# Performance work log

Hardware: AMD Instinct MI355X
Metric: run time of the kernel (lower is better)

## Reference

```python
import jax, jax.numpy as jnp
import numpy as np

B, N, M, G = 2, 8192, 8192, 256
X_MIN = Y_MIN = -35.0
CELL = abs(2.0 * X_MIN / G)  # cell size, as in construct_batched_cuda_grid


def setup_inputs() -> dict:
    key = jax.random.key(0)
    k1, k2, k3, k4, k5 = jax.random.split(key, 5)
    p_i = jax.random.uniform(k1, (B, N, 3), jnp.float32, -34.0, 34.0)
    p_j = jax.random.uniform(k2, (B, M, 3), jnp.float32, -34.0, 34.0)
    mos = jax.random.normal(k3, (B, 2, G, G), jnp.float32)
    error_p_i_flow = jax.random.uniform(k4, (B, N), jnp.float32)
    nearest_flow = jax.random.randint(k5, (B, N, 1), 0, M, jnp.int32)
    return {"p_i": p_i, "mos": mos, "p_j": p_j,
            "error_p_i_flow": error_p_i_flow, "nearest_flow": nearest_flow}


def _knn1_l1(x, y):
    # brute-force 1-NN with L1 (norm=1) distance, matching knn_points(..., K=1, norm=1)
    # build (B,N,M) dist one coordinate at a time to avoid a (B,N,M,3) intermediate
    d = (jnp.abs(x[:, :, None, 0] - y[:, None, :, 0])
         + jnp.abs(x[:, :, None, 1] - y[:, None, :, 1])
         + jnp.abs(x[:, :, None, 2] - y[:, None, :, 2]))
    return jnp.min(d, axis=-1), jnp.argmin(d, axis=-1)


def reference(p_i, mos, p_j, error_p_i_flow, nearest_flow):
    # NN_loss with reduction='none' -> error_p_i_rigid = (cham_x + cham_y)/2 (needs N==M)
    cham_x, nearest_rigid = _knn1_l1(p_i, p_j)  # (B,N), (B,N)
    cham_y, _ = _knn1_l1(p_j, p_i)              # (B,M)
    error_p_i_rigid = (cham_x + cham_y) * 0.5

    dynamic = error_p_i_flow > error_p_i_rigid             # (B,N) bool
    idx = jnp.where(dynamic, nearest_flow[..., 0], nearest_rigid)  # (B,N)
    art_labels = dynamic.astype(jnp.int32)                 # (B,N) in {0,1}

    # batched gather p_j[b, idx[b]]
    p_j_by_nn = jnp.take_along_axis(p_j, idx[..., None], axis=1)  # (B,N,3)

    # construct_batched_cuda_grid: scatter labels into (B,G,G), -1 elsewhere
    shift = jnp.array([X_MIN, Y_MIN], jnp.float32)
    cell_idx = ((p_j_by_nn[:, :, :2] - shift) / CELL).astype(jnp.int32)  # (B,N,2)
    bs = jnp.repeat(jnp.arange(B), N)
    grid = -jnp.ones((B, G, G), jnp.int32)
    grid = grid.at[bs,
                   cell_idx[..., 0].reshape(-1),
                   cell_idx[..., 1].reshape(-1)].set(art_labels.reshape(-1))

    # CrossEntropyLoss(ignore_index=-1), mean over non-ignored cells
    logp = jax.nn.log_softmax(mos, axis=1)                 # (B,C,G,G)
    valid = grid >= 0
    tgt = jnp.clip(grid, 0, None)
    lp = jnp.take_along_axis(logp, tgt[:, None], axis=1)[:, 0]  # (B,G,G)
    loss = -jnp.where(valid, lp, 0.0).sum() / jnp.maximum(valid.sum(), 1).astype(lp.dtype)
    return loss
```

## Files before the change

### kernel.cpp

```cpp
#include <hip/hip_runtime.h>
#include <float.h>

#define B_ 2
#define N_ 8192
#define G_ 256
constexpr float X_MIN_F = -35.0f;
constexpr float CELL_F  = 0.2734375f;

using u64 = unsigned long long;

#define OFF_ACCUM 524288
#define OFF_PX    524352

template<int CC>
__global__ __launch_bounds__(256) void nn_kernel(const float* __restrict__ p_i,
                                                 const float* __restrict__ p_j,
                                                 u64* __restrict__ px,
                                                 float* __restrict__ py,
                                                 int* __restrict__ grid,
                                                 unsigned* __restrict__ accum)
{
    constexpr int COLS = N_ / CC;
    constexpr int NB   = 32 * CC;
    const int dir  = blockIdx.z >> 1;
    const int b    = blockIdx.z & 1;
    const int tid  = threadIdx.x;
    const int row0 = blockIdx.x * 1024 + tid * 4;
    const int c0   = blockIdx.y * COLS;

    const float* __restrict__ P = dir ? p_j : p_i;
    const float* __restrict__ Q = dir ? p_i : p_j;

    __shared__ __align__(16) float q[COLS * 3];
    for (int t = tid; t < COLS * 3 / 4; t += 256)
        ((float4*)q)[t] = ((const float4*)(Q + ((size_t)b * N_ + c0) * 3))[t];

    {
        const int lin = blockIdx.x + 8 * (blockIdx.y + CC * blockIdx.z);
        constexpr int PER = 32768 / NB;
        if (tid < PER)
            ((uint4*)grid)[lin * PER + tid] = make_uint4(~0u, ~0u, ~0u, ~0u);
        if (lin == 0 && tid < 4) accum[tid] = 0u;
    }

    const float4* pp = (const float4*)(P + ((size_t)b * N_ + row0) * 3);
    float4 r0 = pp[0], r1 = pp[1], r2 = pp[2];
    float px_[4] = {r0.x, r0.w, r1.z, r2.y};
    float py_[4] = {r0.y, r1.x, r1.w, r2.z};
    float pz_[4] = {r0.z, r1.y, r2.x, r2.w};

    float best[4];
#pragma unroll
    for (int r = 0; r < 4; r++) best[r] = FLT_MAX;

    __syncthreads();

    if (dir == 0) {
        int gcol[4] = {0, 0, 0, 0};
        for (int jg = 0; jg < COLS; jg += 8) {
            const float4* qv = (const float4*)&q[jg * 3];
            float4 v0 = qv[0], v1 = qv[1], v2 = qv[2];
            float4 v3 = qv[3], v4 = qv[4], v5 = qv[5];
            float qx[8] = {v0.x, v0.w, v1.z, v2.y, v3.x, v3.w, v4.z, v5.y};
            float qy[8] = {v0.y, v1.x, v1.w, v2.z, v3.y, v4.x, v4.w, v5.z};
            float qz[8] = {v0.z, v1.y, v2.x, v2.w, v3.z, v4.y, v5.x, v5.w};
#pragma unroll
            for (int r = 0; r < 4; r++) {
                float d[8];
#pragma unroll
                for (int k = 0; k < 8; k++)
                    d[k] = (fabsf(px_[r] - qx[k]) + fabsf(py_[r] - qy[k]))
                           + fabsf(pz_[r] - qz[k]);
                float m01 = fminf(d[0], d[1]), m23 = fminf(d[2], d[3]);
                float m45 = fminf(d[4], d[5]), m67 = fminf(d[6], d[7]);
                float m = fminf(fminf(m01, m23), fminf(m45, m67));
                bool lt = m < best[r];
                best[r] = lt ? m : best[r];
                gcol[r] = lt ? jg : gcol[r];
            }
        }
        int bidx[4];
#pragma unroll
        for (int r = 0; r < 4; r++) {
            const float4* qv = (const float4*)&q[gcol[r] * 3];
            float4 v0 = qv[0], v1 = qv[1], v2 = qv[2];
            float4 v3 = qv[3], v4 = qv[4], v5 = qv[5];
            float qx[8] = {v0.x, v0.w, v1.z, v2.y, v3.x, v3.w, v4.z, v5.y};
            float qy[8] = {v0.y, v1.x, v1.w, v2.z, v3.y, v4.x, v4.w, v5.z};
            float qz[8] = {v0.z, v1.y, v2.x, v2.w, v3.z, v4.y, v5.x, v5.w};
            int kk = 0;
#pragma unroll
            for (int k = 7; k >= 0; k--) {
                float d = (fabsf(px_[r] - qx[k]) + fabsf(py_[r] - qy[k]))
                          + fabsf(pz_[r] - qz[k]);
                kk = (d == best[r]) ? k : kk;
            }
            bidx[r] = c0 + gcol[r] + kk;
        }
        const size_t o = (size_t)blockIdx.y * (B_ * N_) + b * N_ + row0;
#pragma unroll
        for (int r = 0; r < 4; r++)
            px[o + r] = ((u64)__float_as_uint(best[r]) << 32) | (unsigned)bidx[r];
    } else {
        for (int jg = 0; jg < COLS; jg += 8) {
            const float4* qv = (const float4*)&q[jg * 3];
            float4 v0 = qv[0], v1 = qv[1], v2 = qv[2];
            float4 v3 = qv[3], v4 = qv[4], v5 = qv[5];
            float qx[8] = {v0.x, v0.w, v1.z, v2.y, v3.x, v3.w, v4.z, v5.y};
            float qy[8] = {v0.y, v1.x, v1.w, v2.z, v3.y, v4.x, v4.w, v5.z};
            float qz[8] = {v0.z, v1.y, v2.x, v2.w, v3.z, v4.y, v5.x, v5.w};
#pragma unroll
            for (int r = 0; r < 4; r++) {
#pragma unroll
                for (int k = 0; k < 8; k++) {
                    float d = (fabsf(px_[r] - qx[k]) + fabsf(py_[r] - qy[k]))
                              + fabsf(pz_[r] - qz[k]);
                    best[r] = fminf(best[r], d);
                }
            }
        }
        const size_t o = (size_t)blockIdx.y * (B_ * N_) + b * N_ + row0;
#pragma unroll
        for (int r = 0; r < 4; r++) py[o + r] = best[r];
    }
}

template<int CC>
__global__ __launch_bounds__(256) void reduce_scatter_kernel(
    const u64* __restrict__ px, const float* __restrict__ py,
    const float* __restrict__ flow, const int* __restrict__ nflow,
    const float* __restrict__ Pj, int* __restrict__ grid)
{
    __shared__ u64      sbx[64];
    __shared__ unsigned sby[64];
    const int tid = threadIdx.x;
    const int p   = tid & 63;
    const int g   = tid >> 6;
    constexpr int CPG = CC / 4;

    if (tid < 64) { sbx[tid] = ~0ull; sby[tid] = ~0u; }
    __syncthreads();

    const int pt = blockIdx.x * 64 + p;
    u64   bx = ~0ull;
    float by = FLT_MAX;
#pragma unroll
    for (int k = 0; k < CPG; k++) {
        int c = g * CPG + k;
        u64 v = px[(size_t)c * (B_ * N_) + pt];
        bx = v < bx ? v : bx;
        by = fminf(by, py[(size_t)c * (B_ * N_) + pt]);
    }
    atomicMin(&sbx[p], bx);
    atomicMin(&sby[p], __float_as_uint(by));
    __syncthreads();

    if (tid < 64) {
        u64 fx = sbx[tid];
        float dx = __uint_as_float((unsigned)(fx >> 32));
        float dy = __uint_as_float(sby[tid]);
        float rigid = (dx + dy) * 0.5f;

        const int i = blockIdx.x * 64 + tid;
        const int b = i >> 13;
        const int n = i & (N_ - 1);

        bool dyn  = flow[i] > rigid;
        int label = dyn ? 1 : 0;
        int idx   = dyn ? nflow[i] : (int)(unsigned)(fx & 0xFFFFFFFFull);

        const float* qp = Pj + ((size_t)b * N_ + idx) * 3;
        float xx = qp[0], yy = qp[1];

        int cx = (int)((xx - X_MIN_F) / CELL_F);
        int cy = (int)((yy - X_MIN_F) / CELL_F);

        atomicMax(&grid[(b << 16) + cx * G_ + cy], (n << 1) | label);
    }
}

__global__ __launch_bounds__(256) void ce_kernel(const float* __restrict__ mos,
                                                 const int* __restrict__ grid,
                                                 float* __restrict__ accum,
                                                 float* __restrict__ out)
{
    int i = blockIdx.x * 256 + threadIdx.x;
    float lsum = 0.0f;
    int   lcnt = 0;

    int packed = grid[i];
    if (packed >= 0) {
        int b    = i >> 16;
        int cell = i & 0xFFFF;
        float m0 = mos[((size_t)b * 2 + 0) * 65536 + cell];
        float m1 = mos[((size_t)b * 2 + 1) * 65536 + cell];
        float mx = fmaxf(m0, m1);
        float lse = logf(expf(m0 - mx) + expf(m1 - mx));
        float sh  = ((packed & 1) ? m1 : m0) - mx;
        lsum = sh - lse;
        lcnt = 1;
    }

#pragma unroll
    for (int o = 32; o > 0; o >>= 1) {
        lsum += __shfl_down(lsum, o);
        lcnt += __shfl_down(lcnt, o);
    }
    __shared__ float wsum[4];
    __shared__ int   wcnt[4];
    int wave = threadIdx.x >> 6;
    if ((threadIdx.x & 63) == 0) { wsum[wave] = lsum; wcnt[wave] = lcnt; }
    __syncthreads();
    if (threadIdx.x == 0) {
        float s = wsum[0] + wsum[1] + wsum[2] + wsum[3];
        int   c = wcnt[0] + wcnt[1] + wcnt[2] + wcnt[3];
        atomicAdd(&accum[0], s);
        atomicAdd((int*)&accum[1], c);
        __threadfence();
        unsigned t = atomicAdd((unsigned*)&accum[2], 1u);
        if (t == gridDim.x - 1) {
            float S = atomicAdd(&accum[0], 0.0f);
            int   C = atomicAdd((int*)&accum[1], 0);
            out[0] = -S / (float)(C > 0 ? C : 1);
        }
    }
}

template<int CC>
static void run(const float* p_i, const float* mos, const float* p_j,
                const float* flow, const int* nflow, float* out,
                char* ws, hipStream_t stream)
{
    int*   grid  = (int*)ws;
    float* accum = (float*)(ws + OFF_ACCUM);
    u64*   px    = (u64*)(ws + OFF_PX);
    float* py    = (float*)(ws + OFF_PX + (size_t)CC * B_ * N_ * 8);

    dim3 g(8, CC, 4);
    nn_kernel<CC><<<g, 256, 0, stream>>>(p_i, p_j, px, py, (int*)grid,
                                         (unsigned*)accum);
    reduce_scatter_kernel<CC><<<256, 256, 0, stream>>>(px, py, flow, nflow,
                                                       p_j, grid);
    ce_kernel<<<(B_ * G_ * G_) / 256, 256, 0, stream>>>(mos, grid, accum, out);
}

extern "C" void kernel_launch(void* const* d_in, const int* in_sizes, int n_in,
                              void* d_out, int out_size, void* d_ws, size_t ws_size,
                              hipStream_t stream)
{
    const float* p_i   = (const float*)d_in[0];
    const float* mos   = (const float*)d_in[1];
    const float* p_j   = (const float*)d_in[2];
    const float* flow  = (const float*)d_in[3];
    const int*   nflow = (const int*)d_in[4];
    float* out = (float*)d_out;
    char* ws = (char*)d_ws;

    if (ws_size >= OFF_PX + (size_t)64 * B_ * N_ * 12)
        run<64>(p_i, mos, p_j, flow, nflow, out, ws, stream);
    else if (ws_size >= OFF_PX + (size_t)32 * B_ * N_ * 12)
        run<32>(p_i, mos, p_j, flow, nflow, out, ws, stream);
    else
        run<8>(p_i, mos, p_j, flow, nflow, out, ws, stream);
}
```

Measured before the change: 128.4 us.

## Use packed float2 math and 8 rows per thread in NN kernel

The brute-force L1 nearest-neighbour kernel now gives each thread 8 query rows instead of 4, which halves the number of row blocks and gets more reuse from each shared-memory column load. The distance math uses 2-wide float vectors so the compiler can emit packed FP32 instructions (v_pk_add/min style) on CDNA. The reduce-scatter kernel is rebalanced to 16 points per block with more column groups per point, and the fallback CC becomes 16 so the smaller grid still divides evenly. The cost is higher register pressure from 8 rows and vector accumulators, plus fewer blocks in the NN launch, which may lower occupancy.

```diff
diff --git a/kernel.cpp b/kernel.cpp
--- a/kernel.cpp
+++ b/kernel.cpp
@@ -8,9 +8,14 @@
 constexpr float CELL_F  = 0.2734375f;
 
 using u64 = unsigned long long;
+typedef float v2f __attribute__((ext_vector_type(2)));
 
 #define OFF_ACCUM 524288
 #define OFF_PX    524352
+
+__device__ __forceinline__ v2f vabs2(v2f x) {
+    return __builtin_elementwise_max(x, -x);
+}
 
 template<int CC>
 __global__ __launch_bounds__(256) void nn_kernel(const float* __restrict__ p_i,
@@ -21,11 +26,11 @@
                                                  unsigned* __restrict__ accum)
 {
     constexpr int COLS = N_ / CC;
-    constexpr int NB   = 32 * CC;
+    constexpr int NB   = 16 * CC;
     const int dir  = blockIdx.z >> 1;
     const int b    = blockIdx.z & 1;
     const int tid  = threadIdx.x;
-    const int row0 = blockIdx.x * 1024 + tid * 4;
+    const int row0 = blockIdx.x * 2048 + tid * 8;
     const int c0   = blockIdx.y * COLS;
 
     const float* __restrict__ P = dir ? p_j : p_i;
@@ -36,52 +41,62 @@
         ((float4*)q)[t] = ((const float4*)(Q + ((size_t)b * N_ + c0) * 3))[t];
 
     {
-        const int lin = blockIdx.x + 8 * (blockIdx.y + CC * blockIdx.z);
+        const int lin = blockIdx.x + 4 * (blockIdx.y + CC * blockIdx.z);
         constexpr int PER = 32768 / NB;
-        if (tid < PER)
-            ((uint4*)grid)[lin * PER + tid] = make_uint4(~0u, ~0u, ~0u, ~0u);
+        for (int t = tid; t < PER; t += 256)
+            ((uint4*)grid)[lin * PER + t] = make_uint4(~0u, ~0u, ~0u, ~0u);
         if (lin == 0 && tid < 4) accum[tid] = 0u;
     }
 
-    const float4* pp = (const float4*)(P + ((size_t)b * N_ + row0) * 3);
-    float4 r0 = pp[0], r1 = pp[1], r2 = pp[2];
-    float px_[4] = {r0.x, r0.w, r1.z, r2.y};
-    float py_[4] = {r0.y, r1.x, r1.w, r2.z};
-    float pz_[4] = {r0.z, r1.y, r2.x, r2.w};
-
-    float best[4];
-#pragma unroll
-    for (int r = 0; r < 4; r++) best[r] = FLT_MAX;
+    float px_[8], py_[8], pz_[8];
+    {
+        const float4* pp = (const float4*)(P + ((size_t)b * N_ + row0) * 3);
+        float4 v0 = pp[0], v1 = pp[1], v2 = pp[2];
+        float4 v3 = pp[3], v4 = pp[4], v5 = pp[5];
+        float X[8] = {v0.x, v0.w, v1.z, v2.y, v3.x, v3.w, v4.z, v5.y};
+        float Y[8] = {v0.y, v1.x, v1.w, v2.z, v3.y, v4.x, v4.w, v5.z};
+        float Z[8] = {v0.z, v1.y, v2.x, v2.w, v3.z, v4.y, v5.x, v5.w};
+#pragma unroll
+        for (int r = 0; r < 8; r++) { px_[r] = X[r]; py_[r] = Y[r]; pz_[r] = Z[r]; }
+    }
 
     __syncthreads();
 
     if (dir == 0) {
-        int gcol[4] = {0, 0, 0, 0};
+        float best[8]; int gcol[8];
+#pragma unroll
+        for (int r = 0; r < 8; r++) { best[r] = FLT_MAX; gcol[r] = 0; }
+
         for (int jg = 0; jg < COLS; jg += 8) {
             const float4* qv = (const float4*)&q[jg * 3];
             float4 v0 = qv[0], v1 = qv[1], v2 = qv[2];
             float4 v3 = qv[3], v4 = qv[4], v5 = qv[5];
-            float qx[8] = {v0.x, v0.w, v1.z, v2.y, v3.x, v3.w, v4.z, v5.y};
-            float qy[8] = {v0.y, v1.x, v1.w, v2.z, v3.y, v4.x, v4.w, v5.z};
-            float qz[8] = {v0.z, v1.y, v2.x, v2.w, v3.z, v4.y, v5.x, v5.w};
-#pragma unroll
-            for (int r = 0; r < 4; r++) {
-                float d[8];
-#pragma unroll
-                for (int k = 0; k < 8; k++)
-                    d[k] = (fabsf(px_[r] - qx[k]) + fabsf(py_[r] - qy[k]))
-                           + fabsf(pz_[r] - qz[k]);
-                float m01 = fminf(d[0], d[1]), m23 = fminf(d[2], d[3]);
-                float m45 = fminf(d[4], d[5]), m67 = fminf(d[6], d[7]);
-                float m = fminf(fminf(m01, m23), fminf(m45, m67));
+            v2f qx2[4] = {{v0.x, v0.w}, {v1.z, v2.y}, {v3.x, v3.w}, {v4.z, v5.y}};
+            v2f qy2[4] = {{v0.y, v1.x}, {v1.w, v2.z}, {v3.y, v4.x}, {v4.w, v5.z}};
+            v2f qz2[4] = {{v0.z, v1.y}, {v2.x, v2.w}, {v3.z, v4.y}, {v5.x, v5.w}};
+#pragma unroll
+            for (int r = 0; r < 8; r++) {
+                v2f P2x = {px_[r], px_[r]};
+                v2f P2y = {py_[r], py_[r]};
+                v2f P2z = {pz_[r], pz_[r]};
+                v2f s[4];
+#pragma unroll
+                for (int t = 0; t < 4; t++) {
+                    s[t] = (vabs2(P2x - qx2[t]) + vabs2(P2y - qy2[t]))
+                           + vabs2(P2z - qz2[t]);
+                }
+                v2f m2 = __builtin_elementwise_min(
+                             __builtin_elementwise_min(s[0], s[1]),
+                             __builtin_elementwise_min(s[2], s[3]));
+                float m = fminf(m2.x, m2.y);
                 bool lt = m < best[r];
                 best[r] = lt ? m : best[r];
                 gcol[r] = lt ? jg : gcol[r];
             }
         }
-        int bidx[4];
-#pragma unroll
-        for (int r = 0; r < 4; r++) {
+        const size_t o = (size_t)blockIdx.y * (B_ * N_) + b * N_ + row0;
+#pragma unroll
+        for (int r = 0; r < 8; r++) {
             const float4* qv = (const float4*)&q[gcol[r] * 3];
             float4 v0 = qv[0], v1 = qv[1], v2 = qv[2];
             float4 v3 = qv[3], v4 = qv[4], v5 = qv[5];
@@ -95,33 +110,37 @@
                           + fabsf(pz_[r] - qz[k]);
                 kk = (d == best[r]) ? k : kk;
             }
-            bidx[r] = c0 + gcol[r] + kk;
-        }
-        const size_t o = (size_t)blockIdx.y * (B_ * N_) + b * N_ + row0;
-#pragma unroll
-        for (int r = 0; r < 4; r++)
-            px[o + r] = ((u64)__float_as_uint(best[r]) << 32) | (unsigned)bidx[r];
+            int bidx = c0 + gcol[r] + kk;
+            px[o + r] = ((u64)__float_as_uint(best[r]) << 32) | (unsigned)bidx;
+        }
     } else {
+        v2f bm[8];
+#pragma unroll
+        for (int r = 0; r < 8; r++) bm[r] = (v2f){FLT_MAX, FLT_MAX};
+
         for (int jg = 0; jg < COLS; jg += 8) {
             const float4* qv = (const float4*)&q[jg * 3];
             float4 v0 = qv[0], v1 = qv[1], v2 = qv[2];
             float4 v3 = qv[3], v4 = qv[4], v5 = qv[5];
-            float qx[8] = {v0.x, v0.w, v1.z, v2.y, v3.x, v3.w, v4.z, v5.y};
-            float qy[8] = {v0.y, v1.x, v1.w, v2.z, v3.y, v4.x, v4.w, v5.z};
-            float qz[8] = {v0.z, v1.y, v2.x, v2.w, v3.z, v4.y, v5.x, v5.w};
-#pragma unroll
-            for (int r = 0; r < 4; r++) {
-#pragma unroll
-                for (int k = 0; k < 8; k++) {
-                    float d = (fabsf(px_[r] - qx[k]) + fabsf(py_[r] - qy[k]))
-                              + fabsf(pz_[r] - qz[k]);
-                    best[r] = fminf(best[r], d);
+            v2f qx2[4] = {{v0.x, v0.w}, {v1.z, v2.y}, {v3.x, v3.w}, {v4.z, v5.y}};
+            v2f qy2[4] = {{v0.y, v1.x}, {v1.w, v2.z}, {v3.y, v4.x}, {v4.w, v5.z}};
+            v2f qz2[4] = {{v0.z, v1.y}, {v2.x, v2.w}, {v3.z, v4.y}, {v5.x, v5.w}};
+#pragma unroll
+            for (int r = 0; r < 8; r++) {
+                v2f P2x = {px_[r], px_[r]};
+                v2f P2y = {py_[r], py_[r]};
+                v2f P2z = {pz_[r], pz_[r]};
+#pragma unroll
+                for (int t = 0; t < 4; t++) {
+                    v2f s = (vabs2(P2x - qx2[t]) + vabs2(P2y - qy2[t]))
+                            + vabs2(P2z - qz2[t]);
+                    bm[r] = __builtin_elementwise_min(bm[r], s);
                 }
             }
         }
         const size_t o = (size_t)blockIdx.y * (B_ * N_) + b * N_ + row0;
 #pragma unroll
-        for (int r = 0; r < 4; r++) py[o + r] = best[r];
+        for (int r = 0; r < 8; r++) py[o + r] = fminf(bm[r].x, bm[r].y);
     }
 }
 
@@ -131,17 +150,17 @@
     const float* __restrict__ flow, const int* __restrict__ nflow,
     const float* __restrict__ Pj, int* __restrict__ grid)
 {
-    __shared__ u64      sbx[64];
-    __shared__ unsigned sby[64];
+    __shared__ u64      sbx[16];
+    __shared__ unsigned sby[16];
     const int tid = threadIdx.x;
-    const int p   = tid & 63;
-    const int g   = tid >> 6;
-    constexpr int CPG = CC / 4;
-
-    if (tid < 64) { sbx[tid] = ~0ull; sby[tid] = ~0u; }
-    __syncthreads();
-
-    const int pt = blockIdx.x * 64 + p;
+    const int p   = tid & 15;
+    const int g   = tid >> 4;
+    constexpr int CPG = CC / 16;
+
+    if (tid < 16) { sbx[tid] = ~0ull; sby[tid] = ~0u; }
+    __syncthreads();
+
+    const int pt = blockIdx.x * 16 + p;
     u64   bx = ~0ull;
     float by = FLT_MAX;
 #pragma unroll
@@ -155,13 +174,13 @@
     atomicMin(&sby[p], __float_as_uint(by));
     __syncthreads();
 
-    if (tid < 64) {
+    if (tid < 16) {
         u64 fx = sbx[tid];
         float dx = __uint_as_float((unsigned)(fx >> 32));
         float dy = __uint_as_float(sby[tid]);
         float rigid = (dx + dy) * 0.5f;
 
-        const int i = blockIdx.x * 64 + tid;
+        const int i = blockIdx.x * 16 + tid;
         const int b = i >> 13;
         const int n = i & (N_ - 1);
 
@@ -236,11 +255,11 @@
     u64*   px    = (u64*)(ws + OFF_PX);
     float* py    = (float*)(ws + OFF_PX + (size_t)CC * B_ * N_ * 8);
 
-    dim3 g(8, CC, 4);
+    dim3 g(4, CC, 4);
     nn_kernel<CC><<<g, 256, 0, stream>>>(p_i, p_j, px, py, (int*)grid,
                                          (unsigned*)accum);
-    reduce_scatter_kernel<CC><<<256, 256, 0, stream>>>(px, py, flow, nflow,
-                                                       p_j, grid);
+    reduce_scatter_kernel<CC><<<(B_ * N_) / 16, 256, 0, stream>>>(
+        px, py, flow, nflow, p_j, grid);
     ce_kernel<<<(B_ * G_ * G_) / 256, 256, 0, stream>>>(mos, grid, accum, out);
 }
 
@@ -261,5 +280,5 @@
     else if (ws_size >= OFF_PX + (size_t)32 * B_ * N_ * 12)
         run<32>(p_i, mos, p_j, flow, nflow, out, ws, stream);
     else
-        run<8>(p_i, mos, p_j, flow, nflow, out, ws, stream);
-}
+        run<16>(p_i, mos, p_j, flow, nflow, out, ws, stream);
+}
```

Result: slower. 145.1 us (+13.0%).

## Reduce partial nearest-neighbour results with global atomics instead of staging buffers

Applied to the files above, without the earlier changes.

The nearest-neighbour kernel now folds each column chunk's result straight into per-point minima in global memory with 64-bit and 32-bit atomicMin, in place of writing CC partial buffers that a separate kernel then reduced. The scatter kernel becomes a simple per-point pass, and the template dispatch on workspace size is removed so the chunk count is fixed at 64. The aim is to cut partial-buffer traffic and the reduction work. In exchange it adds a memset to initialise the minima and 64-way atomic contention per point.

```diff
diff --git a/kernel.cpp b/kernel.cpp
--- a/kernel.cpp
+++ b/kernel.cpp
@@ -9,19 +9,18 @@
 
 using u64 = unsigned long long;
 
-#define OFF_ACCUM 524288
-#define OFF_PX    524352
-
-template<int CC>
+#define OFF_CHAMY 131072
+#define OFF_GRID  196608
+#define OFF_ACCUM 720896
+
 __global__ __launch_bounds__(256) void nn_kernel(const float* __restrict__ p_i,
                                                  const float* __restrict__ p_j,
-                                                 u64* __restrict__ px,
-                                                 float* __restrict__ py,
+                                                 u64* __restrict__ chamx,
+                                                 unsigned* __restrict__ chamy,
                                                  int* __restrict__ grid,
                                                  unsigned* __restrict__ accum)
 {
-    constexpr int COLS = N_ / CC;
-    constexpr int NB   = 32 * CC;
+    constexpr int COLS = 128;
     const int dir  = blockIdx.z >> 1;
     const int b    = blockIdx.z & 1;
     const int tid  = threadIdx.x;
@@ -32,14 +31,13 @@
     const float* __restrict__ Q = dir ? p_i : p_j;
 
     __shared__ __align__(16) float q[COLS * 3];
-    for (int t = tid; t < COLS * 3 / 4; t += 256)
-        ((float4*)q)[t] = ((const float4*)(Q + ((size_t)b * N_ + c0) * 3))[t];
+    if (tid < COLS * 3 / 4)
+        ((float4*)q)[tid] = ((const float4*)(Q + ((size_t)b * N_ + c0) * 3))[tid];
 
     {
-        const int lin = blockIdx.x + 8 * (blockIdx.y + CC * blockIdx.z);
-        constexpr int PER = 32768 / NB;
-        if (tid < PER)
-            ((uint4*)grid)[lin * PER + tid] = make_uint4(~0u, ~0u, ~0u, ~0u);
+        const int lin = blockIdx.x + 8 * (blockIdx.y + 64 * blockIdx.z);
+        if (tid < 16)
+            ((uint4*)grid)[lin * 16 + tid] = make_uint4(~0u, ~0u, ~0u, ~0u);
         if (lin == 0 && tid < 4) accum[tid] = 0u;
     }
 
@@ -79,7 +77,6 @@
                 gcol[r] = lt ? jg : gcol[r];
             }
         }
-        int bidx[4];
 #pragma unroll
         for (int r = 0; r < 4; r++) {
             const float4* qv = (const float4*)&q[gcol[r] * 3];
@@ -95,12 +92,10 @@
                           + fabsf(pz_[r] - qz[k]);
                 kk = (d == best[r]) ? k : kk;
             }
-            bidx[r] = c0 + gcol[r] + kk;
-        }
-        const size_t o = (size_t)blockIdx.y * (B_ * N_) + b * N_ + row0;
-#pragma unroll
-        for (int r = 0; r < 4; r++)
-            px[o + r] = ((u64)__float_as_uint(best[r]) << 32) | (unsigned)bidx[r];
+            int bidx = c0 + gcol[r] + kk;
+            u64 pk = ((u64)__float_as_uint(best[r]) << 32) | (unsigned)bidx;
+            atomicMin(&chamx[(size_t)b * N_ + row0 + r], pk);
+        }
     } else {
         for (int jg = 0; jg < COLS; jg += 8) {
             const float4* qv = (const float4*)&q[jg * 3];
@@ -119,64 +114,38 @@
                 }
             }
         }
-        const size_t o = (size_t)blockIdx.y * (B_ * N_) + b * N_ + row0;
-#pragma unroll
-        for (int r = 0; r < 4; r++) py[o + r] = best[r];
-    }
-}
-
-template<int CC>
-__global__ __launch_bounds__(256) void reduce_scatter_kernel(
-    const u64* __restrict__ px, const float* __restrict__ py,
+#pragma unroll
+        for (int r = 0; r < 4; r++)
+            atomicMin(&chamy[(size_t)b * N_ + row0 + r],
+                      __float_as_uint(best[r]));
+    }
+}
+
+__global__ __launch_bounds__(256) void scatter_kernel(
+    const u64* __restrict__ chamx, const unsigned* __restrict__ chamy,
     const float* __restrict__ flow, const int* __restrict__ nflow,
     const float* __restrict__ Pj, int* __restrict__ grid)
 {
-    __shared__ u64      sbx[64];
-    __shared__ unsigned sby[64];
-    const int tid = threadIdx.x;
-    const int p   = tid & 63;
-    const int g   = tid >> 6;
-    constexpr int CPG = CC / 4;
-
-    if (tid < 64) { sbx[tid] = ~0ull; sby[tid] = ~0u; }
-    __syncthreads();
-
-    const int pt = blockIdx.x * 64 + p;
-    u64   bx = ~0ull;
-    float by = FLT_MAX;
-#pragma unroll
-    for (int k = 0; k < CPG; k++) {
-        int c = g * CPG + k;
-        u64 v = px[(size_t)c * (B_ * N_) + pt];
-        bx = v < bx ? v : bx;
-        by = fminf(by, py[(size_t)c * (B_ * N_) + pt]);
-    }
-    atomicMin(&sbx[p], bx);
-    atomicMin(&sby[p], __float_as_uint(by));
-    __syncthreads();
-
-    if (tid < 64) {
-        u64 fx = sbx[tid];
-        float dx = __uint_as_float((unsigned)(fx >> 32));
-        float dy = __uint_as_float(sby[tid]);
-        float rigid = (dx + dy) * 0.5f;
-
-        const int i = blockIdx.x * 64 + tid;
-        const int b = i >> 13;
-        const int n = i & (N_ - 1);
-
-        bool dyn  = flow[i] > rigid;
-        int label = dyn ? 1 : 0;
-        int idx   = dyn ? nflow[i] : (int)(unsigned)(fx & 0xFFFFFFFFull);
-
-        const float* qp = Pj + ((size_t)b * N_ + idx) * 3;
-        float xx = qp[0], yy = qp[1];
-
-        int cx = (int)((xx - X_MIN_F) / CELL_F);
-        int cy = (int)((yy - X_MIN_F) / CELL_F);
-
-        atomicMax(&grid[(b << 16) + cx * G_ + cy], (n << 1) | label);
-    }
+    int i = blockIdx.x * 256 + threadIdx.x;
+    int b = i >> 13;
+    int n = i & (N_ - 1);
+
+    u64 pX = chamx[i];
+    float dx = __uint_as_float((unsigned)(pX >> 32));
+    float dy = __uint_as_float(chamy[i]);
+    float rigid = (dx + dy) * 0.5f;
+
+    bool dyn  = flow[i] > rigid;
+    int label = dyn ? 1 : 0;
+    int idx   = dyn ? nflow[i] : (int)(unsigned)(pX & 0xFFFFFFFFull);
+
+    const float* qp = Pj + ((size_t)b * N_ + idx) * 3;
+    float x = qp[0], y = qp[1];
+
+    int cx = (int)((x - X_MIN_F) / CELL_F);
+    int cy = (int)((y - X_MIN_F) / CELL_F);
+
+    atomicMax(&grid[(b << 16) + cx * G_ + cy], (n << 1) | label);
 }
 
 __global__ __launch_bounds__(256) void ce_kernel(const float* __restrict__ mos,
@@ -226,24 +195,6 @@
     }
 }
 
-template<int CC>
-static void run(const float* p_i, const float* mos, const float* p_j,
-                const float* flow, const int* nflow, float* out,
-                char* ws, hipStream_t stream)
-{
-    int*   grid  = (int*)ws;
-    float* accum = (float*)(ws + OFF_ACCUM);
-    u64*   px    = (u64*)(ws + OFF_PX);
-    float* py    = (float*)(ws + OFF_PX + (size_t)CC * B_ * N_ * 8);
-
-    dim3 g(8, CC, 4);
-    nn_kernel<CC><<<g, 256, 0, stream>>>(p_i, p_j, px, py, (int*)grid,
-                                         (unsigned*)accum);
-    reduce_scatter_kernel<CC><<<256, 256, 0, stream>>>(px, py, flow, nflow,
-                                                       p_j, grid);
-    ce_kernel<<<(B_ * G_ * G_) / 256, 256, 0, stream>>>(mos, grid, accum, out);
-}
-
 extern "C" void kernel_launch(void* const* d_in, const int* in_sizes, int n_in,
                               void* d_out, int out_size, void* d_ws, size_t ws_size,
                               hipStream_t stream)
@@ -256,10 +207,17 @@
     float* out = (float*)d_out;
     char* ws = (char*)d_ws;
 
-    if (ws_size >= OFF_PX + (size_t)64 * B_ * N_ * 12)
-        run<64>(p_i, mos, p_j, flow, nflow, out, ws, stream);
-    else if (ws_size >= OFF_PX + (size_t)32 * B_ * N_ * 12)
-        run<32>(p_i, mos, p_j, flow, nflow, out, ws, stream);
-    else
-        run<8>(p_i, mos, p_j, flow, nflow, out, ws, stream);
-}
+    u64*      chamx = (u64*)ws;
+    unsigned* chamy = (unsigned*)(ws + OFF_CHAMY);
+    int*      grid  = (int*)(ws + OFF_GRID);
+    float*    accum = (float*)(ws + OFF_ACCUM);
+
+    hipMemsetAsync(ws, 0xFF, OFF_GRID, stream);
+
+    dim3 g(8, 64, 4);
+    nn_kernel<<<g, 256, 0, stream>>>(p_i, p_j, chamx, chamy, grid,
+                                     (unsigned*)accum);
+    scatter_kernel<<<(B_ * N_) / 256, 256, 0, stream>>>(chamx, chamy, flow,
+                                                        nflow, p_j, grid);
+    ce_kernel<<<(B_ * G_ * G_) / 256, 256, 0, stream>>>(mos, grid, accum, out);
+}
```

Measured after the change: 131.9 us. 1.03x slower.

## Fuse reduce-scatter and cross-entropy kernels with a software grid barrier

Applied to the files above, without the earlier changes.

Merges the reduce/scatter kernel and the cross-entropy kernel into one launch of 256 blocks. A global atomic spin barrier separates the grid scatter from the loss phase, and each block then processes 512 grid cells instead of 256. This removes one kernel launch and its gap, but relies on all 256 blocks being co-resident and depends on the barrier counter being reset (accum[3]) somewhere not visible. The px stores are also moved into the index-resolution loop, and the fallback column split changes from 8 to 16.

```diff
diff --git a/kernel.cpp b/kernel.cpp
--- a/kernel.cpp
+++ b/kernel.cpp
@@ -79,7 +79,7 @@
                 gcol[r] = lt ? jg : gcol[r];
             }
         }
-        int bidx[4];
+        const size_t o = (size_t)blockIdx.y * (B_ * N_) + b * N_ + row0;
 #pragma unroll
         for (int r = 0; r < 4; r++) {
             const float4* qv = (const float4*)&q[gcol[r] * 3];
@@ -95,12 +95,9 @@
                           + fabsf(pz_[r] - qz[k]);
                 kk = (d == best[r]) ? k : kk;
             }
-            bidx[r] = c0 + gcol[r] + kk;
-        }
-        const size_t o = (size_t)blockIdx.y * (B_ * N_) + b * N_ + row0;
-#pragma unroll
-        for (int r = 0; r < 4; r++)
-            px[o + r] = ((u64)__float_as_uint(best[r]) << 32) | (unsigned)bidx[r];
+            int bidx = c0 + gcol[r] + kk;
+            px[o + r] = ((u64)__float_as_uint(best[r]) << 32) | (unsigned)bidx;
+        }
     } else {
         for (int jg = 0; jg < COLS; jg += 8) {
             const float4* qv = (const float4*)&q[jg * 3];
@@ -126,102 +123,119 @@
 }
 
 template<int CC>
-__global__ __launch_bounds__(256) void reduce_scatter_kernel(
+__global__ __launch_bounds__(256) void rsc_kernel(
     const u64* __restrict__ px, const float* __restrict__ py,
     const float* __restrict__ flow, const int* __restrict__ nflow,
-    const float* __restrict__ Pj, int* __restrict__ grid)
+    const float* __restrict__ Pj, const float* __restrict__ mos,
+    int* __restrict__ grid, float* __restrict__ accum,
+    float* __restrict__ out)
 {
     __shared__ u64      sbx[64];
     __shared__ unsigned sby[64];
+    const int bid = blockIdx.x;
     const int tid = threadIdx.x;
-    const int p   = tid & 63;
-    const int g   = tid >> 6;
-    constexpr int CPG = CC / 4;
-
-    if (tid < 64) { sbx[tid] = ~0ull; sby[tid] = ~0u; }
+
+    {
+        const int p = tid & 63;
+        const int g = tid >> 6;
+        constexpr int CPG = CC / 4;
+
+        if (tid < 64) { sbx[tid] = ~0ull; sby[tid] = ~0u; }
+        __syncthreads();
+
+        const int pt = bid * 64 + p;
+        u64   bx = ~0ull;
+        float by = FLT_MAX;
+#pragma unroll 4
+        for (int k = 0; k < CPG; k++) {
+            int c = g * CPG + k;
+            u64 v = px[(size_t)c * (B_ * N_) + pt];
+            bx = v < bx ? v : bx;
+            by = fminf(by, py[(size_t)c * (B_ * N_) + pt]);
+        }
+        atomicMin(&sbx[p], bx);
+        atomicMin(&sby[p], __float_as_uint(by));
+        __syncthreads();
+
+        if (tid < 64) {
+            u64 fx = sbx[tid];
+            float dx = __uint_as_float((unsigned)(fx >> 32));
+            float dy = __uint_as_float(sby[tid]);
+            float rigid = (dx + dy) * 0.5f;
+
+            const int i = bid * 64 + tid;
+            const int b = i >> 13;
+            const int n = i & (N_ - 1);
+
+            bool dyn  = flow[i] > rigid;
+            int label = dyn ? 1 : 0;
+            int idx   = dyn ? nflow[i] : (int)(unsigned)(fx & 0xFFFFFFFFull);
+
+            const float* qp = Pj + ((size_t)b * N_ + idx) * 3;
+            float xx = qp[0], yy = qp[1];
+
+            int cx = (int)((xx - X_MIN_F) / CELL_F);
+            int cy = (int)((yy - X_MIN_F) / CELL_F);
+
+            atomicMax(&grid[(b << 16) + cx * G_ + cy], (n << 1) | label);
+        }
+    }
+
     __syncthreads();
-
-    const int pt = blockIdx.x * 64 + p;
-    u64   bx = ~0ull;
-    float by = FLT_MAX;
-#pragma unroll
-    for (int k = 0; k < CPG; k++) {
-        int c = g * CPG + k;
-        u64 v = px[(size_t)c * (B_ * N_) + pt];
-        bx = v < bx ? v : bx;
-        by = fminf(by, py[(size_t)c * (B_ * N_) + pt]);
-    }
-    atomicMin(&sbx[p], bx);
-    atomicMin(&sby[p], __float_as_uint(by));
+    if (tid == 0) {
+        unsigned* bar = (unsigned*)accum + 3;
+        __threadfence();
+        atomicAdd(bar, 1u);
+        while (__hip_atomic_load(bar, __ATOMIC_RELAXED,
+                                 __HIP_MEMORY_SCOPE_AGENT) < 256u)
+            __builtin_amdgcn_s_sleep(1);
+        __threadfence();
+    }
     __syncthreads();
 
-    if (tid < 64) {
-        u64 fx = sbx[tid];
-        float dx = __uint_as_float((unsigned)(fx >> 32));
-        float dy = __uint_as_float(sby[tid]);
-        float rigid = (dx + dy) * 0.5f;
-
-        const int i = blockIdx.x * 64 + tid;
-        const int b = i >> 13;
-        const int n = i & (N_ - 1);
-
-        bool dyn  = flow[i] > rigid;
-        int label = dyn ? 1 : 0;
-        int idx   = dyn ? nflow[i] : (int)(unsigned)(fx & 0xFFFFFFFFull);
-
-        const float* qp = Pj + ((size_t)b * N_ + idx) * 3;
-        float xx = qp[0], yy = qp[1];
-
-        int cx = (int)((xx - X_MIN_F) / CELL_F);
-        int cy = (int)((yy - X_MIN_F) / CELL_F);
-
-        atomicMax(&grid[(b << 16) + cx * G_ + cy], (n << 1) | label);
-    }
-}
-
-__global__ __launch_bounds__(256) void ce_kernel(const float* __restrict__ mos,
-                                                 const int* __restrict__ grid,
-                                                 float* __restrict__ accum,
-                                                 float* __restrict__ out)
-{
-    int i = blockIdx.x * 256 + threadIdx.x;
-    float lsum = 0.0f;
-    int   lcnt = 0;
-
-    int packed = grid[i];
-    if (packed >= 0) {
-        int b    = i >> 16;
-        int cell = i & 0xFFFF;
-        float m0 = mos[((size_t)b * 2 + 0) * 65536 + cell];
-        float m1 = mos[((size_t)b * 2 + 1) * 65536 + cell];
-        float mx = fmaxf(m0, m1);
-        float lse = logf(expf(m0 - mx) + expf(m1 - mx));
-        float sh  = ((packed & 1) ? m1 : m0) - mx;
-        lsum = sh - lse;
-        lcnt = 1;
-    }
-
-#pragma unroll
-    for (int o = 32; o > 0; o >>= 1) {
-        lsum += __shfl_down(lsum, o);
-        lcnt += __shfl_down(lcnt, o);
-    }
-    __shared__ float wsum[4];
-    __shared__ int   wcnt[4];
-    int wave = threadIdx.x >> 6;
-    if ((threadIdx.x & 63) == 0) { wsum[wave] = lsum; wcnt[wave] = lcnt; }
-    __syncthreads();
-    if (threadIdx.x == 0) {
-        float s = wsum[0] + wsum[1] + wsum[2] + wsum[3];
-        int   c = wcnt[0] + wcnt[1] + wcnt[2] + wcnt[3];
-        atomicAdd(&accum[0], s);
-        atomicAdd((int*)&accum[1], c);
-        __threadfence();
-        unsigned t = atomicAdd((unsigned*)&accum[2], 1u);
-        if (t == gridDim.x - 1) {
-            float S = atomicAdd(&accum[0], 0.0f);
-            int   C = atomicAdd((int*)&accum[1], 0);
-            out[0] = -S / (float)(C > 0 ? C : 1);
+    {
+        float lsum = 0.0f;
+        int   lcnt = 0;
+#pragma unroll
+        for (int h = 0; h < 2; h++) {
+            int i = bid * 512 + h * 256 + tid;
+            int packed = __hip_atomic_load(&grid[i], __ATOMIC_RELAXED,
+                                           __HIP_MEMORY_SCOPE_AGENT);
+            if (packed >= 0) {
+                int b    = i >> 16;
+                int cell = i & 0xFFFF;
+                float m0 = mos[((size_t)b * 2 + 0) * 65536 + cell];
+                float m1 = mos[((size_t)b * 2 + 1) * 65536 + cell];
+                float mx = fmaxf(m0, m1);
+                float lse = logf(expf(m0 - mx) + expf(m1 - mx));
+                float sh  = ((packed & 1) ? m1 : m0) - mx;
+                lsum += sh - lse;
+                lcnt += 1;
+            }
+        }
+
+#pragma unroll
+        for (int o = 32; o > 0; o >>= 1) {
+            lsum += __shfl_down(lsum, o);
+            lcnt += __shfl_down(lcnt, o);
+        }
+        __shared__ float wsum[4];
+        __shared__ int   wcnt[4];
+        int wave = tid >> 6;
+        if ((tid & 63) == 0) { wsum[wave] = lsum; wcnt[wave] = lcnt; }
+        __syncthreads();
+        if (tid == 0) {
+            float s = wsum[0] + wsum[1] + wsum[2] + wsum[3];
+            int   c = wcnt[0] + wcnt[1] + wcnt[2] + wcnt[3];
+            atomicAdd(&accum[0], s);
+            atomicAdd((int*)&accum[1], c);
+            __threadfence();
+            unsigned t = atomicAdd((unsigned*)&accum[2], 1u);
+            if (t == 255u) {
+                float S = atomicAdd(&accum[0], 0.0f);
+                int   C = atomicAdd((int*)&accum[1], 0);
+                out[0] = -S / (float)(C > 0 ? C : 1);
+            }
         }
     }
 }
@@ -237,11 +251,10 @@
     float* py    = (float*)(ws + OFF_PX + (size_t)CC * B_ * N_ * 8);
 
     dim3 g(8, CC, 4);
-    nn_kernel<CC><<<g, 256, 0, stream>>>(p_i, p_j, px, py, (int*)grid,
+    nn_kernel<CC><<<g, 256, 0, stream>>>(p_i, p_j, px, py, grid,
                                          (unsigned*)accum);
-    reduce_scatter_kernel<CC><<<256, 256, 0, stream>>>(px, py, flow, nflow,
-                                                       p_j, grid);
-    ce_kernel<<<(B_ * G_ * G_) / 256, 256, 0, stream>>>(mos, grid, accum, out);
+    rsc_kernel<CC><<<256, 256, 0, stream>>>(px, py, flow, nflow, p_j, mos,
+                                            grid, accum, out);
 }
 
 extern "C" void kernel_launch(void* const* d_in, const int* in_sizes, int n_in,
@@ -261,5 +274,5 @@
     else if (ws_size >= OFF_PX + (size_t)32 * B_ * N_ * 12)
         run<32>(p_i, mos, p_j, flow, nflow, out, ws, stream);
     else
-        run<8>(p_i, mos, p_j, flow, nflow, out, ws, stream);
-}
+        run<16>(p_i, mos, p_j, flow, nflow, out, ws, stream);
+}
```

After: 137.9 us. 7.4% more time.
